# Kernel optimization log

Hardware: AMD Instinct MI355X
Metric: run time of the kernel (lower is better)

## Reference

```python
import jax, jax.numpy as jnp
import numpy as np

K_NEIGHBORS = 5
WEIGHT = 0.5
EPS = 1e-12


def _l2_normalize(x):
    return x / jnp.maximum(jnp.linalg.norm(x, axis=1, keepdims=True), EPS)


def setup_inputs() -> dict:
    key = jax.random.key(0)
    k1, k2, k3, k4 = jax.random.split(key, 4)
    return {
        "hidden_current": jax.random.normal(k1, (4096, 768), dtype=jnp.float32),
        "hidden_previous": jax.random.normal(k2, (8192, 768), dtype=jnp.float32),
        "labels_current": jax.random.randint(k3, (4096,), 0, 100, dtype=jnp.int64),
        "labels_previous": jax.random.randint(k4, (8192,), 0, 100, dtype=jnp.int64),
    }


def reference(hidden_current, hidden_previous, labels_current, labels_previous):
    B_curr = hidden_current.shape[0]
    B_prev = hidden_previous.shape[0]

    # --- affinity from previous representations (no_grad in original) ---
    hp = _l2_normalize(jax.lax.stop_gradient(hidden_previous))
    dist_prev = 1.0 - hp @ hp.T                      # [B_prev, B_prev] cosine distance
    # smallest k+1 distances == largest k+1 of negated distances
    _, nbr = jax.lax.top_k(-dist_prev, K_NEIGHBORS + 1)
    nbr = nbr[:, 1:]                                 # drop self, [B_prev, K]
    same = labels_previous[:, None] == labels_previous[nbr]   # [B_prev, K]
    e = jnp.where(same, 1.0, -1.0).astype(jnp.float32)        # w - b
    rows = jnp.arange(B_prev)[:, None]
    affinity = jnp.zeros((B_prev, B_prev), dtype=jnp.float32).at[rows, nbr].set(e)

    # --- squared pairwise distances of normalized current representations ---
    hc = _l2_normalize(hidden_current)
    sq = jnp.sum(hc * hc, axis=1)
    d2 = jnp.maximum(sq[:, None] + sq[None, :] - 2.0 * (hc @ hc.T), 0.0)  # [B_curr, B_curr]

    loss = jnp.sum(affinity[:B_curr, :B_curr] * d2) / (B_curr * B_curr)
    return WEIGHT * loss
```

## Files before the change

kernel.cpp:

```cpp
#include <hip/hip_runtime.h>

#define BC 4096
#define BP 8192
#define D  768
#define KNB 5
#define TOPK 6
#define NT (BP / 128)

typedef __bf16 bf16x8 __attribute__((ext_vector_type(8)));
typedef float  f32x4  __attribute__((ext_vector_type(4)));

__device__ __forceinline__ unsigned short f2bf(float f) {
    unsigned int u = __float_as_uint(f);
    u += 0x7fffu + ((u >> 16) & 1u);
    return (unsigned short)(u >> 16);
}

__device__ __forceinline__ void gload16(const void* g, void* l) {
    __builtin_amdgcn_global_load_lds(
        (const __attribute__((address_space(1))) unsigned int*)g,
        (__attribute__((address_space(3))) unsigned int*)l, 16, 0, 0);
}

__device__ __forceinline__ void topk_insert_u(unsigned v, unsigned* bk) {
    unsigned c = v;
    #pragma unroll
    for (int q = 0; q < TOPK; q++) {
        unsigned hi = (c > bk[q]) ? c : bk[q];
        c           = (c > bk[q]) ? bk[q] : c;
        bk[q] = hi;
    }
}

__global__ __launch_bounds__(256) void k_norm(const float* __restrict__ hp,
                                              const float* __restrict__ hc,
                                              unsigned short* __restrict__ hpnb,
                                              float* __restrict__ hcn,
                                              float* __restrict__ sqout,
                                              float* __restrict__ out) {
    int b = blockIdx.x;
    int t = threadIdx.x;
    if (b == 0 && t == 0) out[0] = 0.0f;
    bool isP = (b < BP);
    int row = isP ? b : (b - BP);
    const float* xr = (isP ? hp : hc) + (size_t)row * D;
    float4 v = {0.f, 0.f, 0.f, 0.f};
    if (t < 192) v = *(const float4*)(xr + 4 * t);
    float s = v.x * v.x + v.y * v.y + v.z * v.z + v.w * v.w;
    #pragma unroll
    for (int off = 32; off; off >>= 1) s += __shfl_xor(s, off, 64);
    __shared__ float wsum[4];
    if ((t & 63) == 0) wsum[t >> 6] = s;
    __syncthreads();
    float tot = wsum[0] + wsum[1] + wsum[2] + wsum[3];
    float rinv = 1.0f / fmaxf(sqrtf(tot), 1e-12f);
    if (t < 192) {
        if (isP) {
            ushort4 o4;
            o4.x = f2bf(v.x * rinv); o4.y = f2bf(v.y * rinv);
            o4.z = f2bf(v.z * rinv); o4.w = f2bf(v.w * rinv);
            int rx = (row & 7) << 3;
            *(ushort4*)(hpnb + (size_t)row * D + ((4 * t) ^ rx)) = o4;
        } else {
            float4 o = {v.x * rinv, v.y * rinv, v.z * rinv, v.w * rinv};
            *(float4*)(hcn + (size_t)row * D + 4 * t) = o;
            if (t == 0) sqout[row] = tot * rinv * rinv;
        }
    }
}

__global__ __launch_bounds__(256, 4) void k_simtop(const unsigned short* __restrict__ hp,
                                                   float* __restrict__ candv,
                                                   int* __restrict__ candi) {
    __shared__ char smem[36864];
    unsigned short* sA = (unsigned short*)smem;
    unsigned short* sB = sA + 128 * 64;
    unsigned* sK = (unsigned*)smem;
    unsigned* mk = (unsigned*)(smem + 33280);

    const int t = threadIdx.x;
    const int l = t & 63;
    const int w = t >> 6;
    const int l15 = l & 15, quad = l >> 4;
    const int wr = w >> 1, wc = w & 1;

    int ri, ci;
    {
        int b = blockIdx.x;
        int super_id = (((b >> 9) & 3) << 3) | (b & 7);
        int within = (b >> 3) & 63;
        ri = (super_id >> 3) * 8 + (within >> 3);
        ci = (super_id & 7) * 8 + (within & 7);
    }

    const int srow = l >> 3, sch = l & 7;
    const unsigned short* Ag = hp + (size_t)(ri * 128 + w * 32 + srow) * D + sch * 8;
    const unsigned short* Bg = hp + (size_t)(ci * 128 + w * 32 + srow) * D + sch * 8;
    unsigned short* la = sA + (w * 32) * 64;
    unsigned short* lb = sB + (w * 32) * 64;

    f32x4 acc[4][4];
    #pragma unroll
    for (int i = 0; i < 4; i++)
        #pragma unroll
        for (int j = 0; j < 4; j++) acc[i][j] = (f32x4){4.f, 4.f, 4.f, 4.f};

    const int x7  = l15 & 7;
    const int ch0 = (quad ^ x7) * 16;
    const int ch1 = ((quad + 4) ^ x7) * 16;

    for (int kk = 0; kk < D; kk += 64) {
        __syncthreads();
        #pragma unroll
        for (int p = 0; p < 4; p++) {
            gload16(Ag + (size_t)(p * 8) * D + kk, la + (p * 8) * 64);
            gload16(Bg + (size_t)(p * 8) * D + kk, lb + (p * 8) * 64);
        }
        __syncthreads();
        #pragma unroll
        for (int ks = 0; ks < 2; ks++) {
            const int ch = ks ? ch1 : ch0;
            bf16x8 af[4], bfr[4];
            #pragma unroll
            for (int mi = 0; mi < 4; mi++)
                af[mi] = *(const bf16x8*)((const char*)sA + (wr * 64 + mi * 16 + l15) * 128 + ch);
            #pragma unroll
            for (int ni = 0; ni < 4; ni++)
                bfr[ni] = *(const bf16x8*)((const char*)sB + (wc * 64 + ni * 16 + l15) * 128 + ch);
            __builtin_amdgcn_s_setprio(1);
            #pragma unroll
            for (int mi = 0; mi < 4; mi++)
                #pragma unroll
                for (int ni = 0; ni < 4; ni++)
                    acc[mi][ni] = __builtin_amdgcn_mfma_f32_16x16x32_bf16(af[mi], bfr[ni], acc[mi][ni], 0, 0, 0);
            __builtin_amdgcn_s_setprio(0);
        }
    }

    unsigned bk[TOPK];
    #pragma unroll
    for (int s = 0; s < TOPK; s++) bk[s] = 0u;

    const int erow = t & 127, scb = (t >> 7) * 32;
    #pragma unroll
    for (int h = 0; h < 2; h++) {
        __syncthreads();
        if (wc == h) {
            #pragma unroll
            for (int ni = 0; ni < 4; ni++) {
                unsigned pk = (unsigned)(127 - h * 64 - ni * 16 - l15);
                #pragma unroll
                for (int mi = 0; mi < 4; mi++) {
                    int colb = ni * 16 + l15;
                    int rowb = wr * 64 + mi * 16 + quad * 4;
                    f32x4 v = acc[mi][ni];
                    #pragma unroll
                    for (int r = 0; r < 4; r++)
                        sK[(rowb + r) * 65 + colb] =
                            (__float_as_uint(v[r]) & 0xFFFFFF80u) | pk;
                }
            }
        }
        __syncthreads();
        const unsigned* rowp = sK + erow * 65 + scb;
        #pragma unroll
        for (int c = 0; c < 32; c++) topk_insert_u(rowp[c], bk);
    }

    __syncthreads();
    if (t >= 128) {
        #pragma unroll
        for (int s = 0; s < TOPK; s++) mk[(t - 128) * 7 + s] = bk[s];
    }
    __syncthreads();
    if (t < 128) {
        #pragma unroll
        for (int s0 = 0; s0 < TOPK; s0++) topk_insert_u(mk[t * 7 + s0], bk);
        size_t o = ((size_t)(ri * 128 + t) * NT + ci) * TOPK;
        #pragma unroll
        for (int s = 0; s < TOPK; s++) {
            unsigned k = bk[s];
            candv[o + s] = __uint_as_float(k & 0xFFFFFF80u);
            candi[o + s] = ci * 128 + 127 - (int)(k & 127u);
        }
    }
}

__global__ __launch_bounds__(256) void k_mergeloss(const float* __restrict__ candv,
                                                   const int* __restrict__ candi,
                                                   const float* __restrict__ hcn,
                                                   const float* __restrict__ sq,
                                                   const int* __restrict__ labp,
                                                   float* __restrict__ out) {
    __shared__ float bsum[4];
    const int w = threadIdx.x >> 6, lane = threadIdx.x & 63;
    const int i = blockIdx.x * 4 + w;

    const unsigned* cv = (const unsigned*)candv + ((size_t)i * NT + lane) * TOPK;
    const int*      cj = candi + ((size_t)i * NT + lane) * TOPK;
    unsigned kv[TOPK]; int ji[TOPK];
    #pragma unroll
    for (int s = 0; s < TOPK; s++) { kv[s] = cv[s]; ji[s] = cj[s]; }

    int nbrj[TOPK];
    #pragma unroll
    for (int p = 0; p < TOPK; p++) {
        unsigned m = kv[0];
        #pragma unroll
        for (int off = 32; off; off >>= 1) {
            unsigned o = __shfl_xor(m, off, 64);
            m = (o > m) ? o : m;
        }
        unsigned long long tied = __ballot(kv[0] == m);
        int src = __ffsll((unsigned long long)tied) - 1;
        nbrj[p] = __shfl(ji[0], src, 64);
        bool me = (lane == src);
        #pragma unroll
        for (int q = 0; q < TOPK - 1; q++) {
            kv[q] = me ? kv[q + 1] : kv[q];
            ji[q] = me ? ji[q + 1] : ji[q];
        }
        kv[TOPK - 1] = me ? 0u : kv[TOPK - 1];
    }

    const float* hi = hcn + (size_t)i * D;
    float4 h0 = *(const float4*)(hi + lane * 4);
    float4 h1 = *(const float4*)(hi + lane * 4 + 256);
    float4 h2 = *(const float4*)(hi + lane * 4 + 512);
    float sqi = sq[i];
    int li = labp[i];
    float part = 0.f;
    float base = 0.f;
    #pragma unroll
    for (int s = 1; s <= KNB; s++) {
        int j = nbrj[s];
        if (j >= BC) continue;
        const float* hj = hcn + (size_t)j * D;
        float4 g0 = *(const float4*)(hj + lane * 4);
        float4 g1 = *(const float4*)(hj + lane * 4 + 256);
        float4 g2 = *(const float4*)(hj + lane * 4 + 512);
        float d = h0.x * g0.x + h0.y * g0.y + h0.z * g0.z + h0.w * g0.w
                + h1.x * g1.x + h1.y * g1.y + h1.z * g1.z + h1.w * g1.w
                + h2.x * g2.x + h2.y * g2.y + h2.z * g2.z + h2.w * g2.w;
        float e = (li == labp[j]) ? 1.0f : -1.0f;
        part += e * (-2.0f) * d;
        if (lane == 0) base += e * (sqi + sq[j]);
    }
    part += base;
    #pragma unroll
    for (int off = 32; off; off >>= 1) part += __shfl_xor(part, off, 64);
    if (lane == 0) bsum[w] = part;
    __syncthreads();
    if (threadIdx.x == 0) {
        float s = bsum[0] + bsum[1] + bsum[2] + bsum[3];
        unsafeAtomicAdd(out, 0.5f * s / ((float)BC * (float)BC));
    }
}

extern "C" void kernel_launch(void* const* d_in, const int* in_sizes, int n_in,
                              void* d_out, int out_size, void* d_ws, size_t ws_size,
                              hipStream_t stream) {
    const float* hc   = (const float*)d_in[0];
    const float* hp   = (const float*)d_in[1];
    const int*   labp = (const int*)d_in[3];
    float* out = (float*)d_out;

    unsigned short* hpnb = (unsigned short*)d_ws;
    float* hcn  = (float*)(hpnb + (size_t)BP * D);
    float* sq   = hcn + (size_t)BC * D;
    float* candv = sq + BC;
    int*   candi = (int*)(candv + (size_t)BC * NT * TOPK);

    k_norm<<<dim3(BP + BC), dim3(256), 0, stream>>>(hp, hc, hpnb, hcn, sq, out);
    k_simtop<<<dim3(2048), dim3(256), 0, stream>>>(hpnb, candv, candi);
    k_mergeloss<<<dim3(BC / 4), dim3(256), 0, stream>>>(candv, candi, hcn, sq, labp, out);
}
```

Measured before the change: 161.3 us.

## Use one wave per row in normalize and store packed top-k keys only

After: 157.9 us. 1.02x faster.

```diff
diff --git a/kernel.cpp b/kernel.cpp
--- a/kernel.cpp
+++ b/kernel.cpp
@@ -38,40 +38,46 @@
                                               float* __restrict__ hcn,
                                               float* __restrict__ sqout,
                                               float* __restrict__ out) {
-    int b = blockIdx.x;
-    int t = threadIdx.x;
-    if (b == 0 && t == 0) out[0] = 0.0f;
-    bool isP = (b < BP);
-    int row = isP ? b : (b - BP);
-    const float* xr = (isP ? hp : hc) + (size_t)row * D;
-    float4 v = {0.f, 0.f, 0.f, 0.f};
-    if (t < 192) v = *(const float4*)(xr + 4 * t);
-    float s = v.x * v.x + v.y * v.y + v.z * v.z + v.w * v.w;
+    const int t = threadIdx.x;
+    const int l = t & 63;
+    const int row = blockIdx.x * 4 + (t >> 6);
+    if (blockIdx.x == 0 && t == 0) out[0] = 0.0f;
+    const bool isP = (row < BP);
+    const int r = isP ? row : row - BP;
+    const float* xr = (isP ? hp : hc) + (size_t)r * D;
+    float4 v0 = *(const float4*)(xr + 4 * l);
+    float4 v1 = *(const float4*)(xr + 4 * l + 256);
+    float4 v2 = *(const float4*)(xr + 4 * l + 512);
+    float s = v0.x * v0.x + v0.y * v0.y + v0.z * v0.z + v0.w * v0.w
+            + v1.x * v1.x + v1.y * v1.y + v1.z * v1.z + v1.w * v1.w
+            + v2.x * v2.x + v2.y * v2.y + v2.z * v2.z + v2.w * v2.w;
     #pragma unroll
     for (int off = 32; off; off >>= 1) s += __shfl_xor(s, off, 64);
-    __shared__ float wsum[4];
-    if ((t & 63) == 0) wsum[t >> 6] = s;
-    __syncthreads();
-    float tot = wsum[0] + wsum[1] + wsum[2] + wsum[3];
-    float rinv = 1.0f / fmaxf(sqrtf(tot), 1e-12f);
-    if (t < 192) {
-        if (isP) {
-            ushort4 o4;
-            o4.x = f2bf(v.x * rinv); o4.y = f2bf(v.y * rinv);
-            o4.z = f2bf(v.z * rinv); o4.w = f2bf(v.w * rinv);
-            int rx = (row & 7) << 3;
-            *(ushort4*)(hpnb + (size_t)row * D + ((4 * t) ^ rx)) = o4;
-        } else {
-            float4 o = {v.x * rinv, v.y * rinv, v.z * rinv, v.w * rinv};
-            *(float4*)(hcn + (size_t)row * D + 4 * t) = o;
-            if (t == 0) sqout[row] = tot * rinv * rinv;
-        }
+    float rinv = 1.0f / fmaxf(sqrtf(s), 1e-12f);
+    if (isP) {
+        unsigned short* yr = hpnb + (size_t)r * D;
+        int rx = (r & 7) << 3;
+        ushort4 a, b, c;
+        a.x = f2bf(v0.x * rinv); a.y = f2bf(v0.y * rinv);
+        a.z = f2bf(v0.z * rinv); a.w = f2bf(v0.w * rinv);
+        b.x = f2bf(v1.x * rinv); b.y = f2bf(v1.y * rinv);
+        b.z = f2bf(v1.z * rinv); b.w = f2bf(v1.w * rinv);
+        c.x = f2bf(v2.x * rinv); c.y = f2bf(v2.y * rinv);
+        c.z = f2bf(v2.z * rinv); c.w = f2bf(v2.w * rinv);
+        *(ushort4*)(yr + ((4 * l) ^ rx))       = a;
+        *(ushort4*)(yr + ((4 * l + 256) ^ rx)) = b;
+        *(ushort4*)(yr + ((4 * l + 512) ^ rx)) = c;
+    } else {
+        float* yr = hcn + (size_t)r * D;
+        *(float4*)(yr + 4 * l)       = (float4){v0.x * rinv, v0.y * rinv, v0.z * rinv, v0.w * rinv};
+        *(float4*)(yr + 4 * l + 256) = (float4){v1.x * rinv, v1.y * rinv, v1.z * rinv, v1.w * rinv};
+        *(float4*)(yr + 4 * l + 512) = (float4){v2.x * rinv, v2.y * rinv, v2.z * rinv, v2.w * rinv};
+        if (l == 0) sqout[r] = s * rinv * rinv;
     }
 }
 
 __global__ __launch_bounds__(256, 4) void k_simtop(const unsigned short* __restrict__ hp,
-                                                   float* __restrict__ candv,
-                                                   int* __restrict__ candi) {
+                                                   unsigned* __restrict__ candk) {
     __shared__ char smem[36864];
     unsigned short* sA = (unsigned short*)smem;
     unsigned short* sB = sA + 128 * 64;
@@ -178,16 +184,11 @@
         for (int s0 = 0; s0 < TOPK; s0++) topk_insert_u(mk[t * 7 + s0], bk);
         size_t o = ((size_t)(ri * 128 + t) * NT + ci) * TOPK;
         #pragma unroll
-        for (int s = 0; s < TOPK; s++) {
-            unsigned k = bk[s];
-            candv[o + s] = __uint_as_float(k & 0xFFFFFF80u);
-            candi[o + s] = ci * 128 + 127 - (int)(k & 127u);
-        }
-    }
-}
-
-__global__ __launch_bounds__(256) void k_mergeloss(const float* __restrict__ candv,
-                                                   const int* __restrict__ candi,
+        for (int s = 0; s < TOPK; s++) candk[o + s] = bk[s];
+    }
+}
+
+__global__ __launch_bounds__(256) void k_mergeloss(const unsigned* __restrict__ candk,
                                                    const float* __restrict__ hcn,
                                                    const float* __restrict__ sq,
                                                    const int* __restrict__ labp,
@@ -196,11 +197,10 @@
     const int w = threadIdx.x >> 6, lane = threadIdx.x & 63;
     const int i = blockIdx.x * 4 + w;
 
-    const unsigned* cv = (const unsigned*)candv + ((size_t)i * NT + lane) * TOPK;
-    const int*      cj = candi + ((size_t)i * NT + lane) * TOPK;
-    unsigned kv[TOPK]; int ji[TOPK];
-    #pragma unroll
-    for (int s = 0; s < TOPK; s++) { kv[s] = cv[s]; ji[s] = cj[s]; }
+    const unsigned* cv = candk + ((size_t)i * NT + lane) * TOPK;
+    unsigned kv[TOPK];
+    #pragma unroll
+    for (int s = 0; s < TOPK; s++) kv[s] = cv[s];
 
     int nbrj[TOPK];
     #pragma unroll
@@ -213,13 +213,11 @@
         }
         unsigned long long tied = __ballot(kv[0] == m);
         int src = __ffsll((unsigned long long)tied) - 1;
-        nbrj[p] = __shfl(ji[0], src, 64);
+        nbrj[p] = src * 128 + 127 - (int)(m & 127u);
         bool me = (lane == src);
         #pragma unroll
-        for (int q = 0; q < TOPK - 1; q++) {
+        for (int q = 0; q < TOPK - 1; q++)
             kv[q] = me ? kv[q + 1] : kv[q];
-            ji[q] = me ? ji[q + 1] : ji[q];
-        }
         kv[TOPK - 1] = me ? 0u : kv[TOPK - 1];
     }
 
@@ -268,10 +266,9 @@
     unsigned short* hpnb = (unsigned short*)d_ws;
     float* hcn  = (float*)(hpnb + (size_t)BP * D);
     float* sq   = hcn + (size_t)BC * D;
-    float* candv = sq + BC;
-    int*   candi = (int*)(candv + (size_t)BC * NT * TOPK);
-
-    k_norm<<<dim3(BP + BC), dim3(256), 0, stream>>>(hp, hc, hpnb, hcn, sq, out);
-    k_simtop<<<dim3(2048), dim3(256), 0, stream>>>(hpnb, candv, candi);
-    k_mergeloss<<<dim3(BC / 4), dim3(256), 0, stream>>>(candv, candi, hcn, sq, labp, out);
-}
+    unsigned* candk = (unsigned*)(sq + BC);
+
+    k_norm<<<dim3((BP + BC) / 4), dim3(256), 0, stream>>>(hp, hc, hpnb, hcn, sq, out);
+    k_simtop<<<dim3(2048), dim3(256), 0, stream>>>(hpnb, candk);
+    k_mergeloss<<<dim3(BC / 4), dim3(256), 0, stream>>>(candk, hcn, sq, labp, out);
+}
```
